# Kernel optimization log

Measured on AMD Instinct MI355X. Metric: run time of the kernel, lower is better.

## Reference

```python
import jax, jax.numpy as jnp
from jax import lax
import numpy as np

# config constants (must match init_kwargs)
G = 64            # grid_size
N_CH = 16         # n_channels
HID = 128         # hidden_dim
N_FROZEN = 4
N_GROWN = 12
CH_EXIST = 0
CH_ANCH = 1
STREET = 3        # street_levels
UPDATE_SCALE = 0.1
B = 2


def _make_kernels():
    d = np.array([-1.0, 0.0, 1.0], np.float32)
    s = np.array([1.0, 2.0, 1.0], np.float32)
    sx = np.einsum('i,j,k->ijk', s, s, d) / 16.0
    sy = np.einsum('i,j,k->ijk', s, d, s) / 16.0
    sz = np.einsum('i,j,k->ijk', d, s, s) / 16.0
    ident = np.zeros((3, 3, 3), np.float32)
    ident[1, 1, 1] = 1.0
    return jnp.asarray(np.stack([ident, sx, sy, sz], axis=0))  # [4,3,3,3]

_KERNELS = _make_kernels()


def _perceive(x):
    # x: [B,C,D,H,W]; replicate-pad then 4 depthwise 3x3x3 stencils, concat k-major
    C = x.shape[1]
    xp = jnp.pad(x, ((0, 0), (0, 0), (1, 1), (1, 1), (1, 1)), mode='edge')
    outs = []
    for k in range(4):
        w = jnp.tile(_KERNELS[k][None, None], (C, 1, 1, 1, 1))  # [C,1,3,3,3]
        outs.append(lax.conv_general_dilated(
            xp, w, window_strides=(1, 1, 1), padding='VALID',
            dimension_numbers=('NCDHW', 'OIDHW', 'NCDHW'),
            feature_group_count=C))
    return jnp.concatenate(outs, axis=1)  # [B,4C,D,H,W]


def _pw(x, w, b):
    # 1x1x1 conv3d == per-voxel linear
    return jnp.einsum('bcdhw,oc->bodhw', x, w) + b[None, :, None, None, None]


def _legality_field(state):
    existing = state[:, CH_EXIST]   # [B,D,H,W]
    anchors = state[:, CH_ANCH]
    z = jnp.arange(G).reshape(1, G, 1, 1)
    above = (z >= STREET).astype(state.dtype)
    at = (z < STREET).astype(state.dtype)
    pos = above + at * anchors
    return jnp.clip((1.0 - existing) * pos, 0.0, 1.0)


def _step(state, w1, b1, w2, b2, w3, b3):
    perc = _perceive(state)
    h = jax.nn.relu(_pw(perc, w1, b1))
    h = jax.nn.relu(_pw(h, w2, b2))
    delta = _pw(h, w3, b3)  # [B,N_GROWN,D,H,W]  (eval mode: no fire mask)
    grown = jnp.clip(state[:, N_FROZEN:] + UPDATE_SCALE * delta, 0.0, 1.0)
    available = 1.0 - state[:, CH_EXIST:CH_EXIST + 1]
    struct = grown[:, 0:1] * available
    struct = struct * _legality_field(state)[:, None]
    grown_masked = jnp.concatenate([struct, grown[:, 1:]], axis=1)
    return jnp.concatenate([state[:, :N_FROZEN], grown_masked], axis=1)


def setup_inputs() -> dict:
    key = jax.random.key(0)
    ks = jax.random.split(key, 7)
    state = jax.random.uniform(ks[0], (B, N_CH, G, G, G), dtype=jnp.float32)
    w1 = jax.random.normal(ks[1], (HID, 4 * N_CH), dtype=jnp.float32) * 0.05
    b1 = jnp.zeros((HID,), jnp.float32)
    w2 = jax.random.normal(ks[2], (HID, HID), dtype=jnp.float32) * 0.05
    b2 = jnp.zeros((HID,), jnp.float32)
    w3 = jax.random.normal(ks[3], (N_GROWN, HID), dtype=jnp.float32) * 0.02
    b3 = jnp.zeros((N_GROWN,), jnp.float32)
    return {'state': state, 'w1': w1, 'b1': b1, 'w2': w2, 'b2': b2,
            'w3': w3, 'b3': b3, 'steps': 1}


def reference(state, w1, b1, w2, b2, w3, b3, steps):
    for _ in range(steps):
        state = _step(state, w1, b1, w2, b2, w3, b3)
    return state
```

## Files before the change

kernel.cpp:

```cpp
#include <hip/hip_runtime.h>


namespace {

using short8   = __attribute__((ext_vector_type(8))) short;
using ushort4v = __attribute__((ext_vector_type(4))) unsigned short;
using uint4v   = __attribute__((ext_vector_type(4))) unsigned int;
using float4v  = __attribute__((ext_vector_type(4))) float;

__device__ inline unsigned short f2bf(float x) {
    return (unsigned short)((__float_as_uint(x) + 0x8000u) >> 16);
}
__device__ inline unsigned pkbf(float lo, float hi) {
    const unsigned a = __float_as_uint(lo) + 0x8000u;
    const unsigned b = __float_as_uint(hi) + 0x8000u;
    return (a >> 16) | (b & 0xFFFF0000u);
}

__global__ void prep_weights(const float* __restrict__ w1,
                             const float* __restrict__ w2,
                             const float* __restrict__ w3,
                             unsigned short* __restrict__ wsb) {
    const int i = blockIdx.x * 256 + threadIdx.x;
    if (i < 128 * 64)  wsb[i] = f2bf(w1[i]);
    if (i < 128 * 128) wsb[8192 + i] = f2bf(w2[i]);
    if (i < 16 * 128)  wsb[24576 + i] = (i < 12 * 128) ? f2bf(w3[i])
                                                       : (unsigned short)0;
}

constexpr int PSTRIDE = 88;
constexpr int HSTRIDE = 152;
constexpr int LDS_US  = 4 * 64 * HSTRIDE;
static_assert(256 * PSTRIDE <= LDS_US, "P must fit under H");

__global__ __launch_bounds__(256, 2)
void nca_mfma(const float* __restrict__ state,
              const float* __restrict__ b1, const float* __restrict__ b2,
              const float* __restrict__ b3,
              const unsigned short* __restrict__ wsb,
              float* __restrict__ out) {
    __shared__ unsigned short ldsH[LDS_US];

    const unsigned short* w1b = wsb;
    const unsigned short* w2b = wsb + 8192;
    const unsigned short* w3b = wsb + 24576;

    const int tid  = threadIdx.x;
    const int lane = tid & 63;
    const int wv   = tid >> 6;
    const int gv0  = blockIdx.x * 256;

    const int gvp = gv0 + tid;
    const int y = (gvp >> 6) & 63;
    const int z = (gvp >> 12) & 63;
    const int b = gvp >> 18;
    const long bbase = (long)b << 22;
    const int vox = gvp & 262143;

    {
        const int x = lane;
        const int zc[3] = {(z > 0 ? z - 1 : 0) << 12, z << 12,
                           (z < 63 ? z + 1 : 63) << 12};
        const int yc[3] = {(y > 0 ? y - 1 : 0) << 6, y << 6,
                           (y < 63 ? y + 1 : 63) << 6};
        int roff[9];
        #pragma unroll
        for (int i = 0; i < 3; ++i)
            #pragma unroll
            for (int j = 0; j < 3; ++j)
                roff[i * 3 + j] = zc[i] + yc[j] + x;

        const int lm = (lane > 0) ? lane - 1 : 0;
        const int lp = (lane < 63) ? lane + 1 : 63;

        unsigned pid[8], psx[8], psy[8], psz[8];
        float eid = 0.f, esx = 0.f, esy = 0.f, esz = 0.f;

        #pragma unroll
        for (int c = 0; c < 16; ++c) {
            const float* p = state + bbase + ((long)c << 18);
            float v[9];
            #pragma unroll
            for (int k = 0; k < 9; ++k) v[k] = p[roff[k]];

            const float ry0 = v[0] + 2.f * v[1] + v[2];
            const float ry1 = v[3] + 2.f * v[4] + v[5];
            const float ry2 = v[6] + 2.f * v[7] + v[8];
            const float A  = ry0 + 2.f * ry1 + ry2;
            const float By = (v[2] - v[0]) + 2.f * (v[5] - v[3])
                           + (v[8] - v[6]);
            const float Bz = (v[6] - v[0]) + 2.f * (v[7] - v[1])
                           + (v[8] - v[2]);

            const float Am  = __shfl(A,  lm, 64), Ap  = __shfl(A,  lp, 64);
            const float Bym = __shfl(By, lm, 64), Byp = __shfl(By, lp, 64);
            const float Bzm = __shfl(Bz, lm, 64), Bzp = __shfl(Bz, lp, 64);

            const float ident = v[4];
            const float sx = (Ap - Am) * 0.0625f;
            const float sy = (Bym + Byp + 2.f * By) * 0.0625f;
            const float sz = (Bzm + Bzp + 2.f * Bz) * 0.0625f;

            if (c < 4)
                out[bbase + ((long)c << 18) + vox] = ident;

            if (c & 1) {
                pid[c >> 1] = pkbf(eid, ident);
                psx[c >> 1] = pkbf(esx, sx);
                psy[c >> 1] = pkbf(esy, sy);
                psz[c >> 1] = pkbf(esz, sz);
            } else {
                eid = ident; esx = sx; esy = sy; esz = sz;
            }
        }

        unsigned short* Pr = ldsH + tid * PSTRIDE;
        *(uint4v*)&Pr[0]  = uint4v{pid[0], pid[1], pid[2], pid[3]};
        *(uint4v*)&Pr[8]  = uint4v{pid[4], pid[5], pid[6], pid[7]};
        *(uint4v*)&Pr[16] = uint4v{psx[0], psx[1], psx[2], psx[3]};
        *(uint4v*)&Pr[24] = uint4v{psx[4], psx[5], psx[6], psx[7]};
        *(uint4v*)&Pr[32] = uint4v{psy[0], psy[1], psy[2], psy[3]};
        *(uint4v*)&Pr[40] = uint4v{psy[4], psy[5], psy[6], psy[7]};
        *(uint4v*)&Pr[48] = uint4v{psz[0], psz[1], psz[2], psz[3]};
        *(uint4v*)&Pr[56] = uint4v{psz[4], psz[5], psz[6], psz[7]};
    }
    __syncthreads();

    const int n16  = lane & 15;
    const int quad = lane >> 4;
    unsigned short* Hw = ldsH + wv * 64 * HSTRIDE;

    float4v acc[8][4];

    #pragma unroll
    for (int rt = 0; rt < 8; ++rt)
        #pragma unroll
        for (int reg = 0; reg < 4; ++reg) {
            const float bb = b1[rt * 16 + quad * 4 + reg];
            #pragma unroll
            for (int nt = 0; nt < 4; ++nt) acc[rt][nt][reg] = bb;
        }

    short8 bP[4][2];
    #pragma unroll
    for (int nt = 0; nt < 4; ++nt)
        #pragma unroll
        for (int ks = 0; ks < 2; ++ks)
            bP[nt][ks] = *(const short8*)&ldsH[(wv * 64 + nt * 16 + n16) * PSTRIDE
                                               + ks * 32 + quad * 8];
    #pragma unroll
    for (int rt = 0; rt < 8; ++rt)
        #pragma unroll
        for (int ks = 0; ks < 2; ++ks) {
            const short8 a = *(const short8*)&w1b[(rt * 16 + n16) * 64
                                                   + ks * 32 + quad * 8];
            #pragma unroll
            for (int nt = 0; nt < 4; ++nt)
                acc[rt][nt] = __builtin_amdgcn_mfma_f32_16x16x32_bf16(
                    a, bP[nt][ks], acc[rt][nt], 0, 0, 0);
        }

    __syncthreads();

    #pragma unroll
    for (int rt = 0; rt < 8; ++rt)
        #pragma unroll
        for (int nt = 0; nt < 4; ++nt) {
            ushort4v hp;
            #pragma unroll
            for (int reg = 0; reg < 4; ++reg)
                hp[reg] = f2bf(fmaxf(acc[rt][nt][reg], 0.f));
            *(ushort4v*)&Hw[(nt * 16 + n16) * HSTRIDE + rt * 16 + quad * 4] = hp;
        }

    #pragma unroll
    for (int rt = 0; rt < 8; ++rt)
        #pragma unroll
        for (int reg = 0; reg < 4; ++reg) {
            const float bb = b2[rt * 16 + quad * 4 + reg];
            #pragma unroll
            for (int nt = 0; nt < 4; ++nt) acc[rt][nt][reg] = bb;
        }
    #pragma unroll
    for (int s = 0; s < 4; ++s) {
        short8 bh[4];
        #pragma unroll
        for (int nt = 0; nt < 4; ++nt)
            bh[nt] = *(const short8*)&Hw[(nt * 16 + n16) * HSTRIDE
                                          + s * 32 + quad * 8];
        #pragma unroll
        for (int rt = 0; rt < 8; ++rt) {
            const short8 a = *(const short8*)&w2b[(rt * 16 + n16) * 128
                                                   + s * 32 + quad * 8];
            #pragma unroll
            for (int nt = 0; nt < 4; ++nt)
                acc[rt][nt] = __builtin_amdgcn_mfma_f32_16x16x32_bf16(
                    a, bh[nt], acc[rt][nt], 0, 0, 0);
        }
    }

    #pragma unroll
    for (int rt = 0; rt < 8; ++rt)
        #pragma unroll
        for (int nt = 0; nt < 4; ++nt) {
            ushort4v hp;
            #pragma unroll
            for (int reg = 0; reg < 4; ++reg)
                hp[reg] = f2bf(fmaxf(acc[rt][nt][reg], 0.f));
            *(ushort4v*)&Hw[(nt * 16 + n16) * HSTRIDE + rt * 16 + quad * 4] = hp;
        }

    float4v acc3[4];
    #pragma unroll
    for (int reg = 0; reg < 4; ++reg) {
        const int rr = quad * 4 + reg;
        const float bb = (rr < 12) ? b3[rr] : 0.f;
        #pragma unroll
        for (int nt = 0; nt < 4; ++nt) acc3[nt][reg] = bb;
    }
    #pragma unroll
    for (int s = 0; s < 4; ++s) {
        const short8 a = *(const short8*)&w3b[n16 * 128 + s * 32 + quad * 8];
        #pragma unroll
        for (int nt = 0; nt < 4; ++nt) {
            const short8 bh = *(const short8*)&Hw[(nt * 16 + n16) * HSTRIDE
                                                   + s * 32 + quad * 8];
            acc3[nt] = __builtin_amdgcn_mfma_f32_16x16x32_bf16(
                a, bh, acc3[nt], 0, 0, 0);
        }
    }

    #pragma unroll
    for (int nt = 0; nt < 4; ++nt) {
        const int gv = gv0 + wv * 64 + nt * 16 + n16;
        const int vx = gv & 262143;
        const int zz = (gv >> 12) & 63;

        const float s0 = state[bbase + vx];
        const float s1 = state[bbase + (1 << 18) + vx];
        const float avail = 1.f - s0;
        const float pos = (zz >= 3) ? 1.f : s1;
        const float legal = fminf(fmaxf(avail * pos, 0.f), 1.f);

        #pragma unroll
        for (int reg = 0; reg < 4; ++reg) {
            const int rr = quad * 4 + reg;
            if (rr < 12) {
                const long off = bbase + ((long)(4 + rr) << 18) + vx;
                const float cen = state[off];
                float g = cen + 0.1f * acc3[nt][reg];
                g = fminf(fmaxf(g, 0.f), 1.f);
                if (rr == 0) g = g * avail * legal;
                out[off] = g;
            }
        }
    }
}

}

extern "C" void kernel_launch(void* const* d_in, const int* in_sizes, int n_in,
                              void* d_out, int out_size, void* d_ws, size_t ws_size,
                              hipStream_t stream) {
    const float* state = (const float*)d_in[0];
    const float* w1    = (const float*)d_in[1];
    const float* b1    = (const float*)d_in[2];
    const float* w2    = (const float*)d_in[3];
    const float* b2    = (const float*)d_in[4];
    const float* w3    = (const float*)d_in[5];
    const float* b3    = (const float*)d_in[6];
    float* out = (float*)d_out;
    unsigned short* wsb = (unsigned short*)d_ws;

    prep_weights<<<dim3(64), dim3(256), 0, stream>>>(w1, w2, w3, wsb);

    const int total = 2 * 64 * 64 * 64;
    nca_mfma<<<dim3(total / 256), dim3(256), 0, stream>>>(
        state, b1, b2, b3, wsb, out);
}
```

Before: 168.1 us.

## Keep MLP hidden activations in registers via permuted weights, split voxels into halves

Hidden activations now stay in registers between layers. The MFMA accumulator layout is repacked directly into the B-operand layout, and the K dimension of w2/w3 is permuted once in the weight-prep kernel to match. Dropping the LDS round-trip shrinks shared memory to just the perception tile, so occupancy can rise to 3 blocks per CU. Each wave now processes its 64 voxels in two halves of 32 to cap register pressure, which means the w1/w2/w3 fragments are reloaded from global memory twice.

```diff
diff --git a/kernel.cpp b/kernel.cpp
--- a/kernel.cpp
+++ b/kernel.cpp
@@ -3,10 +3,9 @@
 
 namespace {
 
-using short8   = __attribute__((ext_vector_type(8))) short;
-using ushort4v = __attribute__((ext_vector_type(4))) unsigned short;
-using uint4v   = __attribute__((ext_vector_type(4))) unsigned int;
-using float4v  = __attribute__((ext_vector_type(4))) float;
+using short8  = __attribute__((ext_vector_type(8))) short;
+using uint4v  = __attribute__((ext_vector_type(4))) unsigned int;
+using float4v = __attribute__((ext_vector_type(4))) float;
 
 __device__ inline unsigned short f2bf(float x) {
     return (unsigned short)((__float_as_uint(x) + 0x8000u) >> 16);
@@ -15,6 +14,10 @@
     const unsigned a = __float_as_uint(lo) + 0x8000u;
     const unsigned b = __float_as_uint(hi) + 0x8000u;
     return (a >> 16) | (b & 0xFFFF0000u);
+}
+__device__ inline short8 mk8(unsigned a, unsigned b, unsigned c, unsigned d) {
+    uint4v t{a, b, c, d};
+    return *(short8*)&t;
 }
 
 __global__ void prep_weights(const float* __restrict__ w1,
@@ -22,24 +25,29 @@
                              const float* __restrict__ w3,
                              unsigned short* __restrict__ wsb) {
     const int i = blockIdx.x * 256 + threadIdx.x;
-    if (i < 128 * 64)  wsb[i] = f2bf(w1[i]);
-    if (i < 128 * 128) wsb[8192 + i] = f2bf(w2[i]);
-    if (i < 16 * 128)  wsb[24576 + i] = (i < 12 * 128) ? f2bf(w3[i])
-                                                       : (unsigned short)0;
-}
-
-constexpr int PSTRIDE = 88;
-constexpr int HSTRIDE = 152;
-constexpr int LDS_US  = 4 * 64 * HSTRIDE;
-static_assert(256 * PSTRIDE <= LDS_US, "P must fit under H");
-
-__global__ __launch_bounds__(256, 2)
+    if (i < 128 * 64) wsb[i] = f2bf(w1[i]);
+    if (i < 128 * 128) {
+        const int o = i >> 7, kp = i & 127;
+        const int src = (kp & 96) + ((kp & 4) << 2) + (((kp >> 3) & 3) << 2) + (kp & 3);
+        wsb[8192 + i] = f2bf(w2[o * 128 + src]);
+    }
+    if (i < 16 * 128) {
+        const int o = i >> 7, kp = i & 127;
+        const int src = (kp & 96) + ((kp & 4) << 2) + (((kp >> 3) & 3) << 2) + (kp & 3);
+        wsb[24576 + i] = (o < 12) ? f2bf(w3[o * 128 + src]) : (unsigned short)0;
+    }
+}
+
+constexpr int PSTRIDE = 72;
+constexpr int LDS_US  = 256 * PSTRIDE;
+
+__global__ __launch_bounds__(256, 3)
 void nca_mfma(const float* __restrict__ state,
               const float* __restrict__ b1, const float* __restrict__ b2,
               const float* __restrict__ b3,
               const unsigned short* __restrict__ wsb,
               float* __restrict__ out) {
-    __shared__ unsigned short ldsH[LDS_US];
+    __shared__ unsigned short ldsP[LDS_US];
 
     const unsigned short* w1b = wsb;
     const unsigned short* w2b = wsb + 8192;
@@ -87,10 +95,8 @@
             const float ry1 = v[3] + 2.f * v[4] + v[5];
             const float ry2 = v[6] + 2.f * v[7] + v[8];
             const float A  = ry0 + 2.f * ry1 + ry2;
-            const float By = (v[2] - v[0]) + 2.f * (v[5] - v[3])
-                           + (v[8] - v[6]);
-            const float Bz = (v[6] - v[0]) + 2.f * (v[7] - v[1])
-                           + (v[8] - v[2]);
+            const float By = (v[2] - v[0]) + 2.f * (v[5] - v[3]) + (v[8] - v[6]);
+            const float Bz = (v[6] - v[0]) + 2.f * (v[7] - v[1]) + (v[8] - v[2]);
 
             const float Am  = __shfl(A,  lm, 64), Ap  = __shfl(A,  lp, 64);
             const float Bym = __shfl(By, lm, 64), Byp = __shfl(By, lp, 64);
@@ -114,7 +120,7 @@
             }
         }
 
-        unsigned short* Pr = ldsH + tid * PSTRIDE;
+        unsigned short* Pr = ldsP + tid * PSTRIDE;
         *(uint4v*)&Pr[0]  = uint4v{pid[0], pid[1], pid[2], pid[3]};
         *(uint4v*)&Pr[8]  = uint4v{pid[4], pid[5], pid[6], pid[7]};
         *(uint4v*)&Pr[16] = uint4v{psx[0], psx[1], psx[2], psx[3]};
@@ -128,130 +134,117 @@
 
     const int n16  = lane & 15;
     const int quad = lane >> 4;
-    unsigned short* Hw = ldsH + wv * 64 * HSTRIDE;
-
-    float4v acc[8][4];
-
-    #pragma unroll
-    for (int rt = 0; rt < 8; ++rt)
-        #pragma unroll
-        for (int reg = 0; reg < 4; ++reg) {
-            const float bb = b1[rt * 16 + quad * 4 + reg];
-            #pragma unroll
-            for (int nt = 0; nt < 4; ++nt) acc[rt][nt][reg] = bb;
-        }
-
-    short8 bP[4][2];
-    #pragma unroll
-    for (int nt = 0; nt < 4; ++nt)
-        #pragma unroll
-        for (int ks = 0; ks < 2; ++ks)
-            bP[nt][ks] = *(const short8*)&ldsH[(wv * 64 + nt * 16 + n16) * PSTRIDE
-                                               + ks * 32 + quad * 8];
-    #pragma unroll
-    for (int rt = 0; rt < 8; ++rt)
-        #pragma unroll
-        for (int ks = 0; ks < 2; ++ks) {
-            const short8 a = *(const short8*)&w1b[(rt * 16 + n16) * 64
+
+    #pragma unroll 1
+    for (int h = 0; h < 2; ++h) {
+        const int vbase = wv * 64 + h * 32;
+
+        float4v acc[8][2];
+        #pragma unroll
+        for (int rt = 0; rt < 8; ++rt)
+            #pragma unroll
+            for (int reg = 0; reg < 4; ++reg) {
+                const float bb = b1[rt * 16 + quad * 4 + reg];
+                acc[rt][0][reg] = bb;
+                acc[rt][1][reg] = bb;
+            }
+
+        short8 bP[2][2];
+        #pragma unroll
+        for (int nt = 0; nt < 2; ++nt)
+            #pragma unroll
+            for (int ks = 0; ks < 2; ++ks)
+                bP[nt][ks] = *(const short8*)&ldsP[(vbase + nt * 16 + n16) * PSTRIDE
                                                    + ks * 32 + quad * 8];
-            #pragma unroll
-            for (int nt = 0; nt < 4; ++nt)
-                acc[rt][nt] = __builtin_amdgcn_mfma_f32_16x16x32_bf16(
-                    a, bP[nt][ks], acc[rt][nt], 0, 0, 0);
-        }
-
-    __syncthreads();
-
-    #pragma unroll
-    for (int rt = 0; rt < 8; ++rt)
-        #pragma unroll
-        for (int nt = 0; nt < 4; ++nt) {
-            ushort4v hp;
-            #pragma unroll
-            for (int reg = 0; reg < 4; ++reg)
-                hp[reg] = f2bf(fmaxf(acc[rt][nt][reg], 0.f));
-            *(ushort4v*)&Hw[(nt * 16 + n16) * HSTRIDE + rt * 16 + quad * 4] = hp;
-        }
-
-    #pragma unroll
-    for (int rt = 0; rt < 8; ++rt)
-        #pragma unroll
-        for (int reg = 0; reg < 4; ++reg) {
-            const float bb = b2[rt * 16 + quad * 4 + reg];
-            #pragma unroll
-            for (int nt = 0; nt < 4; ++nt) acc[rt][nt][reg] = bb;
-        }
-    #pragma unroll
-    for (int s = 0; s < 4; ++s) {
-        short8 bh[4];
-        #pragma unroll
-        for (int nt = 0; nt < 4; ++nt)
-            bh[nt] = *(const short8*)&Hw[(nt * 16 + n16) * HSTRIDE
-                                          + s * 32 + quad * 8];
-        #pragma unroll
-        for (int rt = 0; rt < 8; ++rt) {
-            const short8 a = *(const short8*)&w2b[(rt * 16 + n16) * 128
-                                                   + s * 32 + quad * 8];
-            #pragma unroll
-            for (int nt = 0; nt < 4; ++nt)
-                acc[rt][nt] = __builtin_amdgcn_mfma_f32_16x16x32_bf16(
-                    a, bh[nt], acc[rt][nt], 0, 0, 0);
-        }
-    }
-
-    #pragma unroll
-    for (int rt = 0; rt < 8; ++rt)
-        #pragma unroll
-        for (int nt = 0; nt < 4; ++nt) {
-            ushort4v hp;
-            #pragma unroll
-            for (int reg = 0; reg < 4; ++reg)
-                hp[reg] = f2bf(fmaxf(acc[rt][nt][reg], 0.f));
-            *(ushort4v*)&Hw[(nt * 16 + n16) * HSTRIDE + rt * 16 + quad * 4] = hp;
-        }
-
-    float4v acc3[4];
-    #pragma unroll
-    for (int reg = 0; reg < 4; ++reg) {
-        const int rr = quad * 4 + reg;
-        const float bb = (rr < 12) ? b3[rr] : 0.f;
-        #pragma unroll
-        for (int nt = 0; nt < 4; ++nt) acc3[nt][reg] = bb;
-    }
-    #pragma unroll
-    for (int s = 0; s < 4; ++s) {
-        const short8 a = *(const short8*)&w3b[n16 * 128 + s * 32 + quad * 8];
-        #pragma unroll
-        for (int nt = 0; nt < 4; ++nt) {
-            const short8 bh = *(const short8*)&Hw[(nt * 16 + n16) * HSTRIDE
-                                                   + s * 32 + quad * 8];
-            acc3[nt] = __builtin_amdgcn_mfma_f32_16x16x32_bf16(
-                a, bh, acc3[nt], 0, 0, 0);
-        }
-    }
-
-    #pragma unroll
-    for (int nt = 0; nt < 4; ++nt) {
-        const int gv = gv0 + wv * 64 + nt * 16 + n16;
-        const int vx = gv & 262143;
-        const int zz = (gv >> 12) & 63;
-
-        const float s0 = state[bbase + vx];
-        const float s1 = state[bbase + (1 << 18) + vx];
-        const float avail = 1.f - s0;
-        const float pos = (zz >= 3) ? 1.f : s1;
-        const float legal = fminf(fmaxf(avail * pos, 0.f), 1.f);
-
+        #pragma unroll
+        for (int rt = 0; rt < 8; ++rt)
+            #pragma unroll
+            for (int ks = 0; ks < 2; ++ks) {
+                const short8 a = *(const short8*)&w1b[(rt * 16 + n16) * 64
+                                                       + ks * 32 + quad * 8];
+                acc[rt][0] = __builtin_amdgcn_mfma_f32_16x16x32_bf16(a, bP[0][ks], acc[rt][0], 0, 0, 0);
+                acc[rt][1] = __builtin_amdgcn_mfma_f32_16x16x32_bf16(a, bP[1][ks], acc[rt][1], 0, 0, 0);
+            }
+
+        unsigned hlo[8][2], hhi[8][2];
+        #pragma unroll
+        for (int rt = 0; rt < 8; ++rt)
+            #pragma unroll
+            for (int nt = 0; nt < 2; ++nt) {
+                hlo[rt][nt] = pkbf(fmaxf(acc[rt][nt][0], 0.f), fmaxf(acc[rt][nt][1], 0.f));
+                hhi[rt][nt] = pkbf(fmaxf(acc[rt][nt][2], 0.f), fmaxf(acc[rt][nt][3], 0.f));
+            }
+
+        float4v acc2[8][2];
+        #pragma unroll
+        for (int rt = 0; rt < 8; ++rt)
+            #pragma unroll
+            for (int reg = 0; reg < 4; ++reg) {
+                const float bb = b2[rt * 16 + quad * 4 + reg];
+                acc2[rt][0][reg] = bb;
+                acc2[rt][1][reg] = bb;
+            }
+        #pragma unroll
+        for (int s = 0; s < 4; ++s) {
+            const short8 bh0 = mk8(hlo[2*s][0], hhi[2*s][0], hlo[2*s+1][0], hhi[2*s+1][0]);
+            const short8 bh1 = mk8(hlo[2*s][1], hhi[2*s][1], hlo[2*s+1][1], hhi[2*s+1][1]);
+            #pragma unroll
+            for (int rt = 0; rt < 8; ++rt) {
+                const short8 a = *(const short8*)&w2b[(rt * 16 + n16) * 128
+                                                       + s * 32 + quad * 8];
+                acc2[rt][0] = __builtin_amdgcn_mfma_f32_16x16x32_bf16(a, bh0, acc2[rt][0], 0, 0, 0);
+                acc2[rt][1] = __builtin_amdgcn_mfma_f32_16x16x32_bf16(a, bh1, acc2[rt][1], 0, 0, 0);
+            }
+        }
+
+        #pragma unroll
+        for (int rt = 0; rt < 8; ++rt)
+            #pragma unroll
+            for (int nt = 0; nt < 2; ++nt) {
+                hlo[rt][nt] = pkbf(fmaxf(acc2[rt][nt][0], 0.f), fmaxf(acc2[rt][nt][1], 0.f));
+                hhi[rt][nt] = pkbf(fmaxf(acc2[rt][nt][2], 0.f), fmaxf(acc2[rt][nt][3], 0.f));
+            }
+
+        float4v acc3[2];
         #pragma unroll
         for (int reg = 0; reg < 4; ++reg) {
             const int rr = quad * 4 + reg;
-            if (rr < 12) {
-                const long off = bbase + ((long)(4 + rr) << 18) + vx;
-                const float cen = state[off];
-                float g = cen + 0.1f * acc3[nt][reg];
-                g = fminf(fmaxf(g, 0.f), 1.f);
-                if (rr == 0) g = g * avail * legal;
-                out[off] = g;
+            const float bb = (rr < 12) ? b3[rr] : 0.f;
+            acc3[0][reg] = bb;
+            acc3[1][reg] = bb;
+        }
+        #pragma unroll
+        for (int s = 0; s < 4; ++s) {
+            const short8 a = *(const short8*)&w3b[n16 * 128 + s * 32 + quad * 8];
+            const short8 bh0 = mk8(hlo[2*s][0], hhi[2*s][0], hlo[2*s+1][0], hhi[2*s+1][0]);
+            const short8 bh1 = mk8(hlo[2*s][1], hhi[2*s][1], hlo[2*s+1][1], hhi[2*s+1][1]);
+            acc3[0] = __builtin_amdgcn_mfma_f32_16x16x32_bf16(a, bh0, acc3[0], 0, 0, 0);
+            acc3[1] = __builtin_amdgcn_mfma_f32_16x16x32_bf16(a, bh1, acc3[1], 0, 0, 0);
+        }
+
+        #pragma unroll
+        for (int nt = 0; nt < 2; ++nt) {
+            const int gv = gv0 + vbase + nt * 16 + n16;
+            const int vx = gv & 262143;
+            const int zz = (gv >> 12) & 63;
+
+            const float s0 = state[bbase + vx];
+            const float s1 = state[bbase + (1 << 18) + vx];
+            const float avail = 1.f - s0;
+            const float pos = (zz >= 3) ? 1.f : s1;
+            const float legal = fminf(fmaxf(avail * pos, 0.f), 1.f);
+
+            #pragma unroll
+            for (int reg = 0; reg < 4; ++reg) {
+                const int rr = quad * 4 + reg;
+                if (rr < 12) {
+                    const long off = bbase + ((long)(4 + rr) << 18) + vx;
+                    const float cen = state[off];
+                    float g = cen + 0.1f * acc3[nt][reg];
+                    g = fminf(fmaxf(g, 0.f), 1.f);
+                    if (rr == 0) g = g * avail * legal;
+                    out[off] = g;
+                }
             }
         }
     }
```

After: 563.9 us. 3.35x slower.
